# Optimization experiments

Measured on AMD Instinct MI355X. Metric: run time of the kernel, lower is better.

Reference implementation:

```python
import jax, jax.numpy as jnp
import numpy as np

TAU = 2.0        # LIFNode default tau
V_TH = 1.0       # v_threshold
BN_EPS = 1e-5


def setup_inputs() -> dict:
    key = jax.random.key(0)
    k1, k2 = jax.random.split(key)
    T, B, C, V, E = 16, 512, 2, 25, 256
    x = jax.random.normal(k1, (T, B, C, V), dtype=jnp.float32)
    W = jax.random.normal(k2, (E, C), dtype=jnp.float32) * 0.5  # conv1x1 weight [out,in]
    gamma = jnp.ones((E,), dtype=jnp.float32)
    beta = jnp.zeros((E,), dtype=jnp.float32)
    return {"x": x, "W": W, "gamma": gamma, "beta": beta}


def reference(x, W, gamma, beta):
    # x: [T, B, C, V]; conv1d(k=1) == channel-mixing matmul
    y = jnp.einsum('tbcv,ec->tbev', x, W)  # [T, B, E, V]
    # BatchNorm1d in training mode: stats over (T*B, V) per channel
    mean = jnp.mean(y, axis=(0, 1, 3), keepdims=True)
    var = jnp.var(y, axis=(0, 1, 3), keepdims=True)
    y = (y - mean) * jax.lax.rsqrt(var + BN_EPS)
    y = y * gamma[None, None, :, None] + beta[None, None, :, None]
    # Multi-step LIF: v += (x - (v - v_reset))/tau; spike = v >= v_th; hard reset to v_reset=0
    v0 = jnp.zeros(y.shape[1:], dtype=y.dtype)  # [B, E, V]
    def step(v, xt):
        v = v + (xt - v) / TAU
        spike = (v >= V_TH).astype(v.dtype)
        v = v * (1.0 - spike)  # hard reset, v_reset = 0
        return v, spike
    _, spikes = jax.lax.scan(step, v0, y)
    return spikes  # [T, B, E, V]
```

## Files before the change

### kernel.cpp

```cpp
#include <hip/hip_runtime.h>
#include <math.h>

constexpr int T = 16, B = 512, C = 2, V = 25, E = 256;
constexpr int EV  = E * V;
constexpr int BEV = B * EV;
constexpr int XT  = B * C * V;
constexpr int NB  = 1600;
constexpr int CHUNKS = 25;
constexpr int BPC = 64;
constexpr int NROWS = 7;
constexpr float NF = 204800.0f;

#define WS_M32(ws) ((float*)(ws))
#define WS_R32(ws) ((float*)(ws) + E)

template<int PASS>
__global__ void __launch_bounds__(256) k_bs(const float* __restrict__ x,
                                            const float* __restrict__ W,
                                            const float* __restrict__ ws,
                                            float* __restrict__ bs) {
    __shared__ float sx[NROWS * 50];
    int p  = blockIdx.x;
    int q0 = p * 128;
    int row_lo = q0 / 25;
    for (int i = threadIdx.x; i < NROWS * 50; i += 256) {
        int r = i / 50;
        if (row_lo + r < 8192) sx[i] = x[(row_lo + r) * 50 + (i - r * 50)];
    }
    __syncthreads();

    int e = threadIdx.x;
    float w0 = W[e * 2 + 0];
    float w1 = W[e * 2 + 1];
    float mn = (PASS == 1) ? WS_M32(ws)[e] : 0.0f;

    int v   = q0 - row_lo * 25;
    int off = v;
    float r[8];
    #pragma unroll
    for (int k = 0; k < 128; k++) {
        float y = __fadd_rn(__fmul_rn(w0, sx[off]), __fmul_rn(w1, sx[off + 25]));
        if (PASS == 1) {
            float d = __fsub_rn(y, mn);
            y = __fmul_rn(d, d);
        }
        int j = k & 7;
        r[j] = (k < 8) ? y : __fadd_rn(r[j], y);
        v++; off++;
        if (v == 25) { v = 0; off += 25; }
    }
    bs[p * 256 + e] =
        __fadd_rn(__fadd_rn(__fadd_rn(r[0], r[1]), __fadd_rn(r[2], r[3])),
                  __fadd_rn(__fadd_rn(r[4], r[5]), __fadd_rn(r[6], r[7])));
}

template<int WHICH>
__global__ void __launch_bounds__(256) k_comb(const float* __restrict__ bs,
                                              float* __restrict__ ws) {
    __shared__ float cb[NB];
    int e = blockIdx.x;
    for (int i = threadIdx.x; i < NB; i += 256) cb[i] = bs[i * 256 + e];
    __syncthreads();
    if (threadIdx.x == 0) {
        float acc = 0.0f;
        for (int c = 0; c < CHUNKS; c++) {
            float t[BPC];
            for (int i = 0; i < BPC; i++) t[i] = cb[c * BPC + i];
            for (int m = BPC / 2; m >= 1; m >>= 1)
                for (int i = 0; i < m; i++)
                    t[i] = __fadd_rn(t[2 * i], t[2 * i + 1]);
            acc = __fadd_rn(acc, t[0]);
        }
        if (WHICH == 0) {
            WS_M32(ws)[e] = __fdiv_rn(acc, NF);
        } else {
            float var = __fdiv_rn(acc, NF);
            WS_R32(ws)[e] = __fdiv_rn(1.0f, __fsqrt_rn(__fadd_rn(var, 1e-5f)));
        }
    }
}

__global__ void __launch_bounds__(256) k_main(const float* __restrict__ x,
                                              const float* __restrict__ W,
                                              const float* __restrict__ g,
                                              const float* __restrict__ bb,
                                              const float* __restrict__ ws,
                                              float* __restrict__ out) {
    int idx = blockIdx.x * 256 + threadIdx.x;
    int b   = idx / EV;
    int rem = idx - b * EV;
    int e   = rem / V;
    int v   = rem - e * V;
    float w0 = W[e * 2 + 0];
    float w1 = W[e * 2 + 1];
    float mn = WS_M32(ws)[e];
    float rs = WS_R32(ws)[e];
    float ga = g[e];
    float be = bb[e];
    int xb = b * (C * V) + v;
    float vm = 0.0f;
    #pragma unroll
    for (int t = 0; t < T; t++) {
        float x0 = x[xb + t * XT];
        float x1 = x[xb + t * XT + V];
        float y = __fadd_rn(__fmul_rn(w0, x0), __fmul_rn(w1, x1));
        y = __fmul_rn(__fsub_rn(y, mn), rs);
        y = __fadd_rn(__fmul_rn(y, ga), be);
        float d = __fmul_rn(__fsub_rn(y, vm), 0.5f);
        vm = __fadd_rn(vm, d);
        bool sp = (vm >= 1.0f);
        out[(size_t)t * BEV + idx] = sp ? 1.0f : 0.0f;
        if (sp) vm = 0.0f;
    }
}

extern "C" void kernel_launch(void* const* d_in, const int* in_sizes, int n_in,
                              void* d_out, int out_size, void* d_ws, size_t ws_size,
                              hipStream_t stream) {
    (void)in_sizes; (void)n_in; (void)out_size; (void)ws_size;
    const float* x  = (const float*)d_in[0];
    const float* W  = (const float*)d_in[1];
    const float* g  = (const float*)d_in[2];
    const float* bb = (const float*)d_in[3];
    float* ws = (float*)d_ws;
    float* bs = (float*)d_out;

    k_bs<0><<<NB, 256, 0, stream>>>(x, W, ws, bs);
    k_comb<0><<<E, 256, 0, stream>>>(bs, ws);
    k_bs<1><<<NB, 256, 0, stream>>>(x, W, ws, bs);
    k_comb<1><<<E, 256, 0, stream>>>(bs, ws);
    k_main<<<BEV / 256, 256, 0, stream>>>(x, W, g, bb, ws, (float*)d_out);
}
```

Before: 264.9 us.

## Parallelize BN stat combine across threads and stage x in shared memory

The combine kernel now splits the per-channel reduction across 25 threads, each tree-summing one 64-element chunk, and thread 0 then adds the chunk sums. This replaces a fully serial single-thread loop, and the rounding order is kept identical. The main kernel stages the 16 timesteps of x for its batch row in shared memory instead of issuing strided global loads per thread. Spike outputs are written with nontemporal stores to reduce cache pollution. Each main block must now fall within a single batch row (256 = 25*EV/... per block), which adds a shared-memory stage and a barrier.

```diff
diff --git a/kernel.cpp b/kernel.cpp
--- a/kernel.cpp
+++ b/kernel.cpp
@@ -55,22 +55,31 @@
 }
 
 template<int WHICH>
-__global__ void __launch_bounds__(256) k_comb(const float* __restrict__ bs,
-                                              float* __restrict__ ws) {
+__global__ void __launch_bounds__(64) k_comb(const float* __restrict__ bs,
+                                             float* __restrict__ ws) {
     __shared__ float cb[NB];
+    __shared__ float csum[CHUNKS];
     int e = blockIdx.x;
-    for (int i = threadIdx.x; i < NB; i += 256) cb[i] = bs[i * 256 + e];
+    for (int i = threadIdx.x; i < NB; i += 64) cb[i] = bs[i * 256 + e];
+    __syncthreads();
+    if (threadIdx.x < CHUNKS) {
+        int c = threadIdx.x;
+        float t[BPC];
+        #pragma unroll
+        for (int i = 0; i < BPC; i++) t[i] = cb[c * BPC + i];
+        #pragma unroll
+        for (int m = BPC / 2; m >= 1; m >>= 1) {
+            #pragma unroll
+            for (int i = 0; i < m; i++)
+                t[i] = __fadd_rn(t[2 * i], t[2 * i + 1]);
+        }
+        csum[c] = t[0];
+    }
     __syncthreads();
     if (threadIdx.x == 0) {
         float acc = 0.0f;
-        for (int c = 0; c < CHUNKS; c++) {
-            float t[BPC];
-            for (int i = 0; i < BPC; i++) t[i] = cb[c * BPC + i];
-            for (int m = BPC / 2; m >= 1; m >>= 1)
-                for (int i = 0; i < m; i++)
-                    t[i] = __fadd_rn(t[2 * i], t[2 * i + 1]);
-            acc = __fadd_rn(acc, t[0]);
-        }
+        #pragma unroll
+        for (int c = 0; c < CHUNKS; c++) acc = __fadd_rn(acc, csum[c]);
         if (WHICH == 0) {
             WS_M32(ws)[e] = __fdiv_rn(acc, NF);
         } else {
@@ -86,9 +95,18 @@
                                               const float* __restrict__ bb,
                                               const float* __restrict__ ws,
                                               float* __restrict__ out) {
-    int idx = blockIdx.x * 256 + threadIdx.x;
-    int b   = idx / EV;
-    int rem = idx - b * EV;
+    __shared__ float sx[T * 50];
+    int blk = blockIdx.x;
+    int b   = blk / 25;
+    int seg = blk - b * 25;
+    for (int i = threadIdx.x; i < T * 50; i += 256) {
+        int t = i / 50;
+        sx[i] = x[b * 50 + t * XT + (i - t * 50)];
+    }
+    __syncthreads();
+
+    int idx = blk * 256 + threadIdx.x;
+    int rem = seg * 256 + threadIdx.x;
     int e   = rem / V;
     int v   = rem - e * V;
     float w0 = W[e * 2 + 0];
@@ -97,19 +115,19 @@
     float rs = WS_R32(ws)[e];
     float ga = g[e];
     float be = bb[e];
-    int xb = b * (C * V) + v;
     float vm = 0.0f;
     #pragma unroll
     for (int t = 0; t < T; t++) {
-        float x0 = x[xb + t * XT];
-        float x1 = x[xb + t * XT + V];
+        float x0 = sx[t * 50 + v];
+        float x1 = sx[t * 50 + 25 + v];
         float y = __fadd_rn(__fmul_rn(w0, x0), __fmul_rn(w1, x1));
         y = __fmul_rn(__fsub_rn(y, mn), rs);
         y = __fadd_rn(__fmul_rn(y, ga), be);
         float d = __fmul_rn(__fsub_rn(y, vm), 0.5f);
         vm = __fadd_rn(vm, d);
         bool sp = (vm >= 1.0f);
-        out[(size_t)t * BEV + idx] = sp ? 1.0f : 0.0f;
+        __builtin_nontemporal_store(sp ? 1.0f : 0.0f,
+                                    &out[(size_t)t * BEV + idx]);
         if (sp) vm = 0.0f;
     }
 }
@@ -126,8 +144,8 @@
     float* bs = (float*)d_out;
 
     k_bs<0><<<NB, 256, 0, stream>>>(x, W, ws, bs);
-    k_comb<0><<<E, 256, 0, stream>>>(bs, ws);
+    k_comb<0><<<E, 64, 0, stream>>>(bs, ws);
     k_bs<1><<<NB, 256, 0, stream>>>(x, W, ws, bs);
-    k_comb<1><<<E, 256, 0, stream>>>(bs, ws);
+    k_comb<1><<<E, 64, 0, stream>>>(bs, ws);
     k_main<<<BEV / 256, 256, 0, stream>>>(x, W, g, bb, ws, (float*)d_out);
 }
```

Result: faster. 257.8 us (-2.7%).
